# Kernel optimization log

Hardware: AMD Instinct MI355X
Metric: run time of the kernel (lower is better)

## Reference

```python
import jax, jax.numpy as jnp
import numpy as np

Q_STAGES = 8      # residual VQ stages
K_CODES = 1024    # codebook size per stage
D = 256           # code dim == encoder channels


def setup_inputs() -> dict:
    key = jax.random.key(0)
    ks = jax.random.split(key, 6)
    B, T = 8, 8192
    x = jax.random.normal(ks[0], (B, 1, T), dtype=jnp.float32)
    enc_w = jax.random.normal(ks[1], (D, 1, 3), dtype=jnp.float32) * 0.3
    enc_b = jnp.zeros((D,), dtype=jnp.float32)
    dec_w = jax.random.normal(ks[2], (1, D, 3), dtype=jnp.float32) * (1.0 / np.sqrt(3 * D))
    dec_b = jnp.zeros((1,), dtype=jnp.float32)
    codebooks = jax.random.normal(ks[3], (Q_STAGES, K_CODES, D), dtype=jnp.float32)
    return {"x": x, "enc_w": enc_w, "enc_b": enc_b,
            "dec_w": dec_w, "dec_b": dec_b, "codebooks": codebooks}


def _conv1d(x, w, b):
    # x: [B,C,T], w: [O,I,3], 'same' padding
    y = jax.lax.conv_general_dilated(x, w, window_strides=(1,), padding='SAME',
                                     dimension_numbers=('NCH', 'OIH', 'NCH'))
    return y + b[None, :, None]


def _rvq(z, codebooks):
    # z: [B,D,T] -> tokens [N,D]
    B, d, T = z.shape
    flat = jnp.transpose(z, (0, 2, 1)).reshape(B * T, d)  # [N,D]

    def stage(carry, cb):
        residual, quant_sum, loss = carry
        r2 = jnp.sum(residual * residual, axis=1, keepdims=True)      # [N,1]
        c2 = jnp.sum(cb * cb, axis=1)                                  # [K]
        dist = r2 - 2.0 * (residual @ cb.T) + c2[None, :]              # [N,K]
        idx = jnp.argmin(dist, axis=1)                                 # [N]
        q = jax.lax.stop_gradient(cb[idx])                             # [N,D]
        loss = loss + jnp.mean((residual - q) ** 2)                    # commitment
        return (residual - q, quant_sum + q, loss), None

    init = (flat, jnp.zeros_like(flat), jnp.float32(0.0))
    (res, quant_sum, loss), _ = jax.lax.scan(stage, init, codebooks)
    # straight-through estimator
    quant = flat + jax.lax.stop_gradient(quant_sum - flat)
    quant = jnp.transpose(quant.reshape(B, T, d), (0, 2, 1))           # [B,D,T]
    return quant, loss


def reference(x, enc_w, enc_b, dec_w, dec_b, codebooks):
    encoded = _conv1d(x, enc_w, enc_b)              # [B,256,T]
    quantized, commit_loss = _rvq(encoded, codebooks)
    decoded = _conv1d(quantized, dec_w, dec_b)      # [B,1,T]
    return decoded, commit_loss
```

## Files before the change

kernel.cpp:

```cpp
#include <hip/hip_runtime.h>

#define QS 8
#define KC 1024
#define DD 256
#define TT 8192
#define NN 65536
#define TAU 0.06f
#define FLAGCAP 49152

typedef _Float16 half8 __attribute__((ext_vector_type(8)));
typedef float f32x4 __attribute__((ext_vector_type(4)));

__device__ __forceinline__ void gload_lds16(const _Float16* g, _Float16* l) {
    __builtin_amdgcn_global_load_lds(
        (const __attribute__((address_space(1))) void*)g,
        (__attribute__((address_space(3))) void*)l,
        16, 0, 0);
}

__global__ __launch_bounds__(256) void encode_init_kernel(
    const float* __restrict__ x, const float* __restrict__ ew,
    const float* __restrict__ eb, float* __restrict__ res,
    float* __restrict__ lossAcc, int* __restrict__ flagCnt)
{
    if (blockIdx.x == 0 && threadIdx.x == 0) *lossAcc = 0.0f;
    if (blockIdx.x == 0 && threadIdx.x < QS) flagCnt[threadIdx.x] = 0;
    const int d = threadIdx.x;
    const float w0 = ew[d*3 + 0];
    const float w1 = ew[d*3 + 1];
    const float w2 = ew[d*3 + 2];
    const float b  = eb[d];
    #pragma unroll 4
    for (int tt = 0; tt < 16; ++tt) {
        const long n = (long)blockIdx.x * 16 + tt;
        const int t = (int)(n & (TT - 1));
        const float xm = (t > 0)      ? x[n - 1] : 0.0f;
        const float x0 = x[n];
        const float xp = (t < TT - 1) ? x[n + 1] : 0.0f;
        res[n * DD + d] = b + w0*xm + w1*x0 + w2*xp;
    }
}

__global__ __launch_bounds__(256) void c2_kernel(
    const float* __restrict__ cbs, float* __restrict__ c2)
{
    const int w = (int)((blockIdx.x * blockDim.x + threadIdx.x) >> 6);
    const int lane = threadIdx.x & 63;
    if (w >= QS * KC) return;
    const float* row = cbs + (long)w * DD;
    float s = 0.0f;
    #pragma unroll
    for (int q = 0; q < DD / 64; ++q) {
        const float v = row[lane + 64*q];
        s += v * v;
    }
    #pragma unroll
    for (int off = 32; off; off >>= 1) s += __shfl_down(s, off, 64);
    if (lane == 0) c2[w] = s;
}

__global__ __launch_bounds__(256) void cb_prep_stage_kernel(
    const float* __restrict__ cb, _Float16* __restrict__ cbh)
{
    const int t = blockIdx.x;
    const int cg = t >> 2, kp = t & 3;
    #pragma unroll
    for (int q = 0; q < 2; ++q) {
        const int p = threadIdx.x + 256*q;
        const int code = p & 63, kchunk = p >> 6;
        const float* src = &cb[(long)(cg*64 + code)*DD + kp*64 + kchunk*8];
        const float4 v0 = *reinterpret_cast<const float4*>(src);
        const float4 v1 = *reinterpret_cast<const float4*>(src + 4);
        half8 hv;
        hv[0]=(_Float16)v0.x; hv[1]=(_Float16)v0.y;
        hv[2]=(_Float16)v0.z; hv[3]=(_Float16)v0.w;
        hv[4]=(_Float16)v1.x; hv[5]=(_Float16)v1.y;
        hv[6]=(_Float16)v1.z; hv[7]=(_Float16)v1.w;
        *reinterpret_cast<half8*>(&cbh[(long)t*4096 + p*8]) = hv;
    }
}

__global__ __launch_bounds__(256, 2) void rvq_pass1_kernel(
    const float* __restrict__ cb,
    const _Float16* __restrict__ cbh,
    const float* __restrict__ c2,
    float* __restrict__ res,
    float* __restrict__ lossAcc,
    int* __restrict__ flagCnt,
    int* __restrict__ flagList)
{
    __shared__ __align__(16) _Float16 Bt[4][4096];
    __shared__ int idxArr[128];

    const int tid = threadIdx.x;
    const int w   = tid >> 6;
    const int l   = tid & 63;
    const int l15 = l & 15;
    const int l4  = l >> 4;
    const long n0 = (long)blockIdx.x * 128;

    int tr;
    {
        half8 pa, pb;
        #pragma unroll
        for (int e = 0; e < 8; ++e) {
            pa[e] = (_Float16)l15;
            pb[e] = (_Float16)0.03125f;
        }
        f32x4 pacc = (f32x4){0.f, 0.f, 0.f, 0.f};
        pacc = __builtin_amdgcn_mfma_f32_16x16x32_f16(pa, pb, pacc, 0, 0, 0);
        const float p1 = __shfl(pacc[1], 0, 64);
        tr = (p1 < 0.5f) ? 1 : 0;
    }

    half8 ah[2][8], al[2][8];
    #pragma unroll
    for (int mt = 0; mt < 2; ++mt) {
      #pragma unroll
      for (int kc = 0; kc < 8; ++kc) {
        const long n = n0 + w*32 + mt*16 + l15;
        const float* p = &res[n*DD + kc*32 + l4*8];
        const float4 v0 = *reinterpret_cast<const float4*>(p);
        const float4 v1 = *reinterpret_cast<const float4*>(p + 4);
        const float xv[8] = {v0.x, v0.y, v0.z, v0.w, v1.x, v1.y, v1.z, v1.w};
        half8 hv, lv;
        #pragma unroll
        for (int e = 0; e < 8; ++e) {
            const _Float16 hh = (_Float16)xv[e];
            hv[e] = hh;
            lv[e] = (_Float16)(xv[e] - (float)hh);
        }
        ah[mt][kc] = hv; al[mt][kc] = lv;
      }
    }

    float b1[8], b2[8]; int i1[8];
    #pragma unroll
    for (int r = 0; r < 8; ++r) { b1[r] = 1e30f; b2[r] = 1e30f; i1[r] = 0; }

    auto stageDMA = [&](int t) {
        const _Float16* src = cbh + (long)t*4096;
        const int buf = t & 3;
        gload_lds16(src + ((w*64 + l)*8),        &Bt[buf][w*512]);
        gload_lds16(src + ((256 + w*64 + l)*8),  &Bt[buf][2048 + w*512]);
    };

    stageDMA(0); stageDMA(1); stageDMA(2);

    for (int cg = 0; cg < 16; ++cg) {
      f32x4 acc[2][4];
      #pragma unroll
      for (int mt = 0; mt < 2; ++mt)
        #pragma unroll
        for (int nt = 0; nt < 4; ++nt)
          acc[mt][nt] = (f32x4){0.f, 0.f, 0.f, 0.f};

      for (int kp = 0; kp < 4; ++kp) {
        const int t = cg*4 + kp, buf = t & 3;

        if (t < 62)       asm volatile("s_waitcnt vmcnt(4)" ::: "memory");
        else if (t == 62) asm volatile("s_waitcnt vmcnt(2)" ::: "memory");
        else              asm volatile("s_waitcnt vmcnt(0)" ::: "memory");
        __builtin_amdgcn_sched_barrier(0);
        __builtin_amdgcn_s_barrier();
        __builtin_amdgcn_sched_barrier(0);

        if (t < 61) stageDMA(t + 3);

        #pragma unroll
        for (int kc2 = 0; kc2 < 2; ++kc2) {
          const int kc = kp*2 + kc2;
          #pragma unroll
          for (int nt = 0; nt < 4; ++nt) {
            const int slot = ((kc2*4 + l4)*64 + nt*16 + l15)*8;
            const half8 bh = *reinterpret_cast<const half8*>(&Bt[buf][slot]);
            #pragma unroll
            for (int mt = 0; mt < 2; ++mt) {
              acc[mt][nt] = __builtin_amdgcn_mfma_f32_16x16x32_f16(ah[mt][kc], bh, acc[mt][nt], 0, 0, 0);
              acc[mt][nt] = __builtin_amdgcn_mfma_f32_16x16x32_f16(al[mt][kc], bh, acc[mt][nt], 0, 0, 0);
            }
          }
        }
      }

      if (tr == 0) {
        #pragma unroll
        for (int nt = 0; nt < 4; ++nt) {
          const int code = cg*64 + nt*16 + l15;
          const float cc = c2[code];
          #pragma unroll
          for (int mt = 0; mt < 2; ++mt) {
            #pragma unroll
            for (int j = 0; j < 4; ++j) {
              const float dist = cc - 2.0f*acc[mt][nt][j];
              const int r = mt*4 + j;
              if (dist < b1[r])      { b2[r] = b1[r]; b1[r] = dist; i1[r] = code; }
              else if (dist < b2[r]) { b2[r] = dist; }
            }
          }
        }
      } else {
        #pragma unroll
        for (int nt = 0; nt < 4; ++nt) {
          #pragma unroll
          for (int j = 0; j < 4; ++j) {
            const int code = cg*64 + nt*16 + l4*4 + j;
            const float cc = c2[code];
            #pragma unroll
            for (int mt = 0; mt < 2; ++mt) {
              const float dist = cc - 2.0f*acc[mt][nt][j];
              if (dist < b1[mt])      { b2[mt] = b1[mt]; b1[mt] = dist; i1[mt] = code; }
              else if (dist < b2[mt]) { b2[mt] = dist; }
            }
          }
        }
      }
    }

    if (tr == 0) {
      #pragma unroll
      for (int m = 1; m < 16; m <<= 1) {
        #pragma unroll
        for (int r = 0; r < 8; ++r) {
          const float ob1 = __shfl_xor(b1[r], m, 64);
          const float ob2 = __shfl_xor(b2[r], m, 64);
          const int   oi1 = __shfl_xor(i1[r], m, 64);
          const float nb2 = fminf(fminf(b2[r], ob2), fmaxf(b1[r], ob1));
          if (ob1 < b1[r] || (ob1 == b1[r] && oi1 < i1[r])) { b1[r] = ob1; i1[r] = oi1; }
          b2[r] = nb2;
        }
      }
      if (l15 == 0) {
        #pragma unroll
        for (int mt = 0; mt < 2; ++mt)
          #pragma unroll
          for (int j = 0; j < 4; ++j) {
            const int r = mt*4 + j;
            const int row = w*32 + mt*16 + l4*4 + j;
            idxArr[row] = i1[r];
            if (b2[r] - b1[r] < TAU) {
              const int pos = atomicAdd(flagCnt, 1);
              if (pos < FLAGCAP)
                flagList[pos] = (int)(((n0 + row) << 10) | (unsigned)i1[r]);
            }
          }
      }
    } else {
      #pragma unroll
      for (int m = 16; m <= 32; m <<= 1) {
        #pragma unroll
        for (int r = 0; r < 2; ++r) {
          const float ob1 = __shfl_xor(b1[r], m, 64);
          const float ob2 = __shfl_xor(b2[r], m, 64);
          const int   oi1 = __shfl_xor(i1[r], m, 64);
          const float nb2 = fminf(fminf(b2[r], ob2), fmaxf(b1[r], ob1));
          if (ob1 < b1[r] || (ob1 == b1[r] && oi1 < i1[r])) { b1[r] = ob1; i1[r] = oi1; }
          b2[r] = nb2;
        }
      }
      if (l4 == 0) {
        #pragma unroll
        for (int mt = 0; mt < 2; ++mt) {
          const int row = w*32 + mt*16 + l15;
          idxArr[row] = i1[mt];
          if (b2[mt] - b1[mt] < TAU) {
            const int pos = atomicAdd(flagCnt, 1);
            if (pos < FLAGCAP)
              flagList[pos] = (int)(((n0 + row) << 10) | (unsigned)i1[mt]);
          }
        }
      }
    }
    __syncthreads();

    float lsum = 0.0f;
    const int rw = tid >> 6;
    const int cc4 = (tid & 63) * 4;
    #pragma unroll 4
    for (int it = 0; it < 32; ++it) {
        const int r = it*4 + rw;
        const long n = n0 + r;
        const int ix = idxArr[r];
        float4 rv = *reinterpret_cast<const float4*>(&res[n*DD + cc4]);
        const float4 cv = *reinterpret_cast<const float4*>(&cb[(long)ix*DD + cc4]);
        rv.x -= cv.x; rv.y -= cv.y; rv.z -= cv.z; rv.w -= cv.w;
        *reinterpret_cast<float4*>(&res[n*DD + cc4]) = rv;
        lsum += rv.x*rv.x + rv.y*rv.y + rv.z*rv.z + rv.w*rv.w;
    }
    #pragma unroll
    for (int off = 32; off; off >>= 1) lsum += __shfl_down(lsum, off, 64);
    if (l == 0) atomicAdd(lossAcc, lsum);
}

__global__ __launch_bounds__(256) void recheck_kernel(
    const float* __restrict__ cb, const float* __restrict__ c2,
    float* __restrict__ res, float* __restrict__ lossAcc,
    const int* __restrict__ flagCnt, const int* __restrict__ flagList)
{
    __shared__ float rorig[DD];
    __shared__ float sD[256];
    __shared__ int   sI[256];
    const int cnt = min(*flagCnt, FLAGCAP);
    const int tid = threadIdx.x;
    for (int f = blockIdx.x; f < cnt; f += gridDim.x) {
        const int packed = flagList[f];
        const long n  = packed >> 10;
        const int old = packed & 1023;
        __syncthreads();
        const float rme = res[n*DD + tid] + cb[(long)old*DD + tid];
        rorig[tid] = rme;
        __syncthreads();
        float bd = 1e30f; int bi = 0;
        #pragma unroll
        for (int q = 0; q < 4; ++q) {
            const int code = tid + 256*q;
            const float* crow = &cb[(long)code*DD];
            float dot = 0.f;
            for (int d = 0; d < DD; ++d) dot += rorig[d]*crow[d];
            const float dist = c2[code] - 2.0f*dot;
            if (dist < bd || (dist == bd && code < bi)) { bd = dist; bi = code; }
        }
        sD[tid] = bd; sI[tid] = bi;
        __syncthreads();
        for (int s = 128; s; s >>= 1) {
            if (tid < s) {
                const float d2 = sD[tid + s]; const int i2 = sI[tid + s];
                if (d2 < sD[tid] || (d2 == sD[tid] && i2 < sI[tid])) { sD[tid] = d2; sI[tid] = i2; }
            }
            __syncthreads();
        }
        const int best = sI[0];
        if (best != old) {
            const float rn = rorig[tid] - cb[(long)best*DD + tid];
            const float ro = res[n*DD + tid];
            res[n*DD + tid] = rn;
            float delta = rn*rn - ro*ro;
            #pragma unroll
            for (int off = 32; off; off >>= 1) delta += __shfl_down(delta, off, 64);
            if ((tid & 63) == 0) atomicAdd(lossAcc, delta);
        }
    }
}

__global__ __launch_bounds__(256) void decode_kernel(
    const float* __restrict__ x,  const float* __restrict__ ew,
    const float* __restrict__ eb, const float* __restrict__ res,
    const float* __restrict__ dw, const float* __restrict__ db,
    const float* __restrict__ lossAcc, float* __restrict__ out)
{
    const long n = (long)blockIdx.x * 4 + (threadIdx.x >> 6);
    const int lane = threadIdx.x & 63;
    const int t = (int)(n & (TT - 1));
    float sum = 0.0f;
    #pragma unroll
    for (int k = 0; k < 3; ++k) {
        const int tm = t + k - 1;
        if (tm < 0 || tm > TT - 1) continue;
        const long m = n + k - 1;
        const float xm = (tm > 0)      ? x[m - 1] : 0.0f;
        const float x0 = x[m];
        const float xp = (tm < TT - 1) ? x[m + 1] : 0.0f;
        #pragma unroll
        for (int q = 0; q < 4; ++q) {
            const int d = lane + 64 * q;
            const float z = eb[d] + ew[d*3]*xm + ew[d*3 + 1]*x0 + ew[d*3 + 2]*xp;
            const float quant = z - res[m * DD + d];
            sum += quant * dw[d*3 + k];
        }
    }
    #pragma unroll
    for (int off = 32; off; off >>= 1) sum += __shfl_down(sum, off, 64);
    if (lane == 0) out[n] = sum + db[0];
    if (blockIdx.x == 0 && threadIdx.x == 0)
        out[NN] = lossAcc[0] * (1.0f / ((float)NN * (float)DD));
}

extern "C" void kernel_launch(void* const* d_in, const int* in_sizes, int n_in,
                              void* d_out, int out_size, void* d_ws, size_t ws_size,
                              hipStream_t stream)
{
    const float* x     = (const float*)d_in[0];
    const float* enc_w = (const float*)d_in[1];
    const float* enc_b = (const float*)d_in[2];
    const float* dec_w = (const float*)d_in[3];
    const float* dec_b = (const float*)d_in[4];
    const float* cbs   = (const float*)d_in[5];
    float* out = (float*)d_out;

    float*    res      = (float*)d_ws;
    float*    lossAcc  = res + (size_t)NN * DD;
    _Float16* cbh      = (_Float16*)(lossAcc + 4);
    int*      flagCnt  = (int*)out;
    float*    c2       = out + 8;
    int*      flagList = (int*)(out + 8 + QS * KC);

    hipLaunchKernelGGL(encode_init_kernel, dim3(NN / 16), dim3(256), 0, stream,
                       x, enc_w, enc_b, res, lossAcc, flagCnt);
    hipLaunchKernelGGL(c2_kernel, dim3(QS * KC / 4), dim3(256), 0, stream,
                       cbs, c2);
    for (int s = 0; s < QS; ++s) {
        hipLaunchKernelGGL(cb_prep_stage_kernel, dim3(64), dim3(256), 0, stream,
                           cbs + (size_t)s * KC * DD, cbh);
        hipLaunchKernelGGL(rvq_pass1_kernel, dim3(NN / 128), dim3(256), 0, stream,
                           cbs + (size_t)s * KC * DD, cbh,
                           c2 + (size_t)s * KC,
                           res, lossAcc, flagCnt + s, flagList);
        hipLaunchKernelGGL(recheck_kernel, dim3(256), dim3(256), 0, stream,
                           cbs + (size_t)s * KC * DD,
                           c2 + (size_t)s * KC,
                           res, lossAcc, flagCnt + s, flagList);
    }
    hipLaunchKernelGGL(decode_kernel, dim3(NN / 4), dim3(256), 0, stream,
                       x, enc_w, enc_b, res, dec_w, dec_b, lossAcc, out);
}
```

Before: 1.507 ms.

## Fuse encoder, all RVQ stages and recheck into one register-resident persistent kernel

Replaces the per-stage prep/pass1/recheck launches with a single kernel. Each thread keeps its token's residual in registers across all eight stages, computes the encoder inline, and handles near-tie rows with an in-block exact fp32 recheck. The final residual is written once in fp16. This removes the repeated global read-modify-write of the 64 MB fp32 residual and about twenty kernel launches. The cost is heavy register pressure from r[8][8] with 512-thread blocks, a serialized in-block recheck loop with many barriers, reduced residual precision going into the decoder, and flags per block capped at 64.

```diff
diff --git a/kernel.cpp b/kernel.cpp
--- a/kernel.cpp
+++ b/kernel.cpp
@@ -6,7 +6,6 @@
 #define TT 8192
 #define NN 65536
 #define TAU 0.06f
-#define FLAGCAP 49152
 
 typedef _Float16 half8 __attribute__((ext_vector_type(8)));
 typedef float f32x4 __attribute__((ext_vector_type(4)));
@@ -18,52 +17,13 @@
         16, 0, 0);
 }
 
-__global__ __launch_bounds__(256) void encode_init_kernel(
-    const float* __restrict__ x, const float* __restrict__ ew,
-    const float* __restrict__ eb, float* __restrict__ res,
-    float* __restrict__ lossAcc, int* __restrict__ flagCnt)
-{
-    if (blockIdx.x == 0 && threadIdx.x == 0) *lossAcc = 0.0f;
-    if (blockIdx.x == 0 && threadIdx.x < QS) flagCnt[threadIdx.x] = 0;
-    const int d = threadIdx.x;
-    const float w0 = ew[d*3 + 0];
-    const float w1 = ew[d*3 + 1];
-    const float w2 = ew[d*3 + 2];
-    const float b  = eb[d];
-    #pragma unroll 4
-    for (int tt = 0; tt < 16; ++tt) {
-        const long n = (long)blockIdx.x * 16 + tt;
-        const int t = (int)(n & (TT - 1));
-        const float xm = (t > 0)      ? x[n - 1] : 0.0f;
-        const float x0 = x[n];
-        const float xp = (t < TT - 1) ? x[n + 1] : 0.0f;
-        res[n * DD + d] = b + w0*xm + w1*x0 + w2*xp;
-    }
-}
-
-__global__ __launch_bounds__(256) void c2_kernel(
-    const float* __restrict__ cbs, float* __restrict__ c2)
-{
-    const int w = (int)((blockIdx.x * blockDim.x + threadIdx.x) >> 6);
-    const int lane = threadIdx.x & 63;
-    if (w >= QS * KC) return;
-    const float* row = cbs + (long)w * DD;
-    float s = 0.0f;
-    #pragma unroll
-    for (int q = 0; q < DD / 64; ++q) {
-        const float v = row[lane + 64*q];
-        s += v * v;
-    }
-    #pragma unroll
-    for (int off = 32; off; off >>= 1) s += __shfl_down(s, off, 64);
-    if (lane == 0) c2[w] = s;
-}
-
-__global__ __launch_bounds__(256) void cb_prep_stage_kernel(
-    const float* __restrict__ cb, _Float16* __restrict__ cbh)
-{
-    const int t = blockIdx.x;
+__global__ __launch_bounds__(256) void cb_prep_all_kernel(
+    const float* __restrict__ cbs, _Float16* __restrict__ cbh)
+{
+    const int b = blockIdx.x, s = b >> 6, t = b & 63;
     const int cg = t >> 2, kp = t & 3;
+    const float* cb = cbs + (size_t)s * KC * DD;
+    _Float16* dst = cbh + (size_t)s * KC * DD + (size_t)t * 4096;
     #pragma unroll
     for (int q = 0; q < 2; ++q) {
         const int p = threadIdx.x + 256*q;
@@ -76,28 +36,51 @@
         hv[2]=(_Float16)v0.z; hv[3]=(_Float16)v0.w;
         hv[4]=(_Float16)v1.x; hv[5]=(_Float16)v1.y;
         hv[6]=(_Float16)v1.z; hv[7]=(_Float16)v1.w;
-        *reinterpret_cast<half8*>(&cbh[(long)t*4096 + p*8]) = hv;
-    }
-}
-
-__global__ __launch_bounds__(256, 2) void rvq_pass1_kernel(
-    const float* __restrict__ cb,
-    const _Float16* __restrict__ cbh,
-    const float* __restrict__ c2,
-    float* __restrict__ res,
-    float* __restrict__ lossAcc,
-    int* __restrict__ flagCnt,
-    int* __restrict__ flagList)
+        *reinterpret_cast<half8*>(&dst[p*8]) = hv;
+    }
+}
+
+__global__ __launch_bounds__(256) void c2_kernel(
+    const float* __restrict__ cbs, float* __restrict__ c2,
+    float* __restrict__ lossAcc)
+{
+    if (blockIdx.x == 0 && threadIdx.x == 0) *lossAcc = 0.0f;
+    const int w = (int)((blockIdx.x * blockDim.x + threadIdx.x) >> 6);
+    const int lane = threadIdx.x & 63;
+    if (w >= QS * KC) return;
+    const float* row = cbs + (long)w * DD;
+    float s = 0.0f;
+    #pragma unroll
+    for (int q = 0; q < DD / 64; ++q) {
+        const float v = row[lane + 64*q];
+        s += v * v;
+    }
+    #pragma unroll
+    for (int off = 32; off; off >>= 1) s += __shfl_down(s, off, 64);
+    if (lane == 0) c2[w] = s;
+}
+
+__global__ __launch_bounds__(512, 2) void mega_kernel(
+    const float* __restrict__ x,   const float* __restrict__ ew,
+    const float* __restrict__ eb,  const float* __restrict__ cbs,
+    const _Float16* __restrict__ cbh, const float* __restrict__ c2,
+    _Float16* __restrict__ resf,   float* __restrict__ lossAcc)
 {
     __shared__ __align__(16) _Float16 Bt[4][4096];
-    __shared__ int idxArr[128];
+    __shared__ int   idxArr[128];
+    __shared__ float rrow[DD];
+    __shared__ float sD8[8];
+    __shared__ int   sI8[8];
+    __shared__ int   flagRows[64];
+    __shared__ int   flagCnt;
 
     const int tid = threadIdx.x;
     const int w   = tid >> 6;
     const int l   = tid & 63;
     const int l15 = l & 15;
     const int l4  = l >> 4;
-    const long n0 = (long)blockIdx.x * 128;
+    const int n0  = blockIdx.x * 128;
+    const int n   = n0 + w*16 + l15;
 
     int tr;
     {
@@ -113,238 +96,226 @@
         tr = (p1 < 0.5f) ? 1 : 0;
     }
 
-    half8 ah[2][8], al[2][8];
-    #pragma unroll
-    for (int mt = 0; mt < 2; ++mt) {
-      #pragma unroll
-      for (int kc = 0; kc < 8; ++kc) {
-        const long n = n0 + w*32 + mt*16 + l15;
-        const float* p = &res[n*DD + kc*32 + l4*8];
-        const float4 v0 = *reinterpret_cast<const float4*>(p);
-        const float4 v1 = *reinterpret_cast<const float4*>(p + 4);
-        const float xv[8] = {v0.x, v0.y, v0.z, v0.w, v1.x, v1.y, v1.z, v1.w};
-        half8 hv, lv;
-        #pragma unroll
-        for (int e = 0; e < 8; ++e) {
-            const _Float16 hh = (_Float16)xv[e];
-            hv[e] = hh;
-            lv[e] = (_Float16)(xv[e] - (float)hh);
-        }
-        ah[mt][kc] = hv; al[mt][kc] = lv;
-      }
-    }
-
-    float b1[8], b2[8]; int i1[8];
-    #pragma unroll
-    for (int r = 0; r < 8; ++r) { b1[r] = 1e30f; b2[r] = 1e30f; i1[r] = 0; }
-
-    auto stageDMA = [&](int t) {
-        const _Float16* src = cbh + (long)t*4096;
-        const int buf = t & 3;
-        gload_lds16(src + ((w*64 + l)*8),        &Bt[buf][w*512]);
-        gload_lds16(src + ((256 + w*64 + l)*8),  &Bt[buf][2048 + w*512]);
-    };
-
-    stageDMA(0); stageDMA(1); stageDMA(2);
-
-    for (int cg = 0; cg < 16; ++cg) {
-      f32x4 acc[2][4];
-      #pragma unroll
-      for (int mt = 0; mt < 2; ++mt)
-        #pragma unroll
-        for (int nt = 0; nt < 4; ++nt)
-          acc[mt][nt] = (f32x4){0.f, 0.f, 0.f, 0.f};
-
-      for (int kp = 0; kp < 4; ++kp) {
-        const int t = cg*4 + kp, buf = t & 3;
-
-        if (t < 62)       asm volatile("s_waitcnt vmcnt(4)" ::: "memory");
-        else if (t == 62) asm volatile("s_waitcnt vmcnt(2)" ::: "memory");
-        else              asm volatile("s_waitcnt vmcnt(0)" ::: "memory");
-        __builtin_amdgcn_sched_barrier(0);
-        __builtin_amdgcn_s_barrier();
-        __builtin_amdgcn_sched_barrier(0);
-
-        if (t < 61) stageDMA(t + 3);
-
-        #pragma unroll
-        for (int kc2 = 0; kc2 < 2; ++kc2) {
-          const int kc = kp*2 + kc2;
-          #pragma unroll
-          for (int nt = 0; nt < 4; ++nt) {
-            const int slot = ((kc2*4 + l4)*64 + nt*16 + l15)*8;
-            const half8 bh = *reinterpret_cast<const half8*>(&Bt[buf][slot]);
-            #pragma unroll
-            for (int mt = 0; mt < 2; ++mt) {
-              acc[mt][nt] = __builtin_amdgcn_mfma_f32_16x16x32_f16(ah[mt][kc], bh, acc[mt][nt], 0, 0, 0);
-              acc[mt][nt] = __builtin_amdgcn_mfma_f32_16x16x32_f16(al[mt][kc], bh, acc[mt][nt], 0, 0, 0);
-            }
-          }
-        }
-      }
-
-      if (tr == 0) {
-        #pragma unroll
-        for (int nt = 0; nt < 4; ++nt) {
-          const int code = cg*64 + nt*16 + l15;
-          const float cc = c2[code];
-          #pragma unroll
-          for (int mt = 0; mt < 2; ++mt) {
-            #pragma unroll
-            for (int j = 0; j < 4; ++j) {
-              const float dist = cc - 2.0f*acc[mt][nt][j];
-              const int r = mt*4 + j;
-              if (dist < b1[r])      { b2[r] = b1[r]; b1[r] = dist; i1[r] = code; }
-              else if (dist < b2[r]) { b2[r] = dist; }
-            }
-          }
-        }
-      } else {
-        #pragma unroll
-        for (int nt = 0; nt < 4; ++nt) {
-          #pragma unroll
-          for (int j = 0; j < 4; ++j) {
-            const int code = cg*64 + nt*16 + l4*4 + j;
-            const float cc = c2[code];
-            #pragma unroll
-            for (int mt = 0; mt < 2; ++mt) {
-              const float dist = cc - 2.0f*acc[mt][nt][j];
-              if (dist < b1[mt])      { b2[mt] = b1[mt]; b1[mt] = dist; i1[mt] = code; }
-              else if (dist < b2[mt]) { b2[mt] = dist; }
-            }
-          }
-        }
-      }
-    }
-
-    if (tr == 0) {
-      #pragma unroll
-      for (int m = 1; m < 16; m <<= 1) {
-        #pragma unroll
-        for (int r = 0; r < 8; ++r) {
-          const float ob1 = __shfl_xor(b1[r], m, 64);
-          const float ob2 = __shfl_xor(b2[r], m, 64);
-          const int   oi1 = __shfl_xor(i1[r], m, 64);
-          const float nb2 = fminf(fminf(b2[r], ob2), fmaxf(b1[r], ob1));
-          if (ob1 < b1[r] || (ob1 == b1[r] && oi1 < i1[r])) { b1[r] = ob1; i1[r] = oi1; }
-          b2[r] = nb2;
-        }
-      }
-      if (l15 == 0) {
-        #pragma unroll
-        for (int mt = 0; mt < 2; ++mt)
-          #pragma unroll
-          for (int j = 0; j < 4; ++j) {
-            const int r = mt*4 + j;
-            const int row = w*32 + mt*16 + l4*4 + j;
-            idxArr[row] = i1[r];
-            if (b2[r] - b1[r] < TAU) {
-              const int pos = atomicAdd(flagCnt, 1);
-              if (pos < FLAGCAP)
-                flagList[pos] = (int)(((n0 + row) << 10) | (unsigned)i1[r]);
-            }
-          }
-      }
-    } else {
-      #pragma unroll
-      for (int m = 16; m <= 32; m <<= 1) {
-        #pragma unroll
-        for (int r = 0; r < 2; ++r) {
-          const float ob1 = __shfl_xor(b1[r], m, 64);
-          const float ob2 = __shfl_xor(b2[r], m, 64);
-          const int   oi1 = __shfl_xor(i1[r], m, 64);
-          const float nb2 = fminf(fminf(b2[r], ob2), fmaxf(b1[r], ob1));
-          if (ob1 < b1[r] || (ob1 == b1[r] && oi1 < i1[r])) { b1[r] = ob1; i1[r] = oi1; }
-          b2[r] = nb2;
-        }
-      }
-      if (l4 == 0) {
-        #pragma unroll
-        for (int mt = 0; mt < 2; ++mt) {
-          const int row = w*32 + mt*16 + l15;
-          idxArr[row] = i1[mt];
-          if (b2[mt] - b1[mt] < TAU) {
-            const int pos = atomicAdd(flagCnt, 1);
-            if (pos < FLAGCAP)
-              flagList[pos] = (int)(((n0 + row) << 10) | (unsigned)i1[mt]);
-          }
-        }
-      }
-    }
-    __syncthreads();
+    float r[8][8];
+    {
+        const int t = n & (TT - 1);
+        const float xm = (t > 0)      ? x[n - 1] : 0.0f;
+        const float x0v = x[n];
+        const float xp = (t < TT - 1) ? x[n + 1] : 0.0f;
+        #pragma unroll
+        for (int kc = 0; kc < 8; ++kc)
+            #pragma unroll
+            for (int e = 0; e < 8; ++e) {
+                const int d = kc*32 + l4*8 + e;
+                r[kc][e] = eb[d] + ew[3*d]*xm + ew[3*d+1]*x0v + ew[3*d+2]*xp;
+            }
+    }
 
     float lsum = 0.0f;
-    const int rw = tid >> 6;
-    const int cc4 = (tid & 63) * 4;
-    #pragma unroll 4
-    for (int it = 0; it < 32; ++it) {
-        const int r = it*4 + rw;
-        const long n = n0 + r;
-        const int ix = idxArr[r];
-        float4 rv = *reinterpret_cast<const float4*>(&res[n*DD + cc4]);
-        const float4 cv = *reinterpret_cast<const float4*>(&cb[(long)ix*DD + cc4]);
-        rv.x -= cv.x; rv.y -= cv.y; rv.z -= cv.z; rv.w -= cv.w;
-        *reinterpret_cast<float4*>(&res[n*DD + cc4]) = rv;
-        lsum += rv.x*rv.x + rv.y*rv.y + rv.z*rv.z + rv.w*rv.w;
+    half8 ah[8], al[8];
+
+    for (int s = 0; s < QS; ++s) {
+        const _Float16* cbhS = cbh + (size_t)s * KC * DD;
+        const float*    cbS  = cbs + (size_t)s * KC * DD;
+        const float*    c2S  = c2 + s * KC;
+
+        #pragma unroll
+        for (int kc = 0; kc < 8; ++kc) {
+            half8 hv, lv;
+            #pragma unroll
+            for (int e = 0; e < 8; ++e) {
+                const _Float16 hh = (_Float16)r[kc][e];
+                hv[e] = hh;
+                lv[e] = (_Float16)(r[kc][e] - (float)hh);
+            }
+            ah[kc] = hv; al[kc] = lv;
+        }
+
+        if (tid == 0) flagCnt = 0;
+
+        float b1[4], b2[4]; int i1[4];
+        #pragma unroll
+        for (int q = 0; q < 4; ++q) { b1[q] = 1e30f; b2[q] = 1e30f; i1[q] = 0; }
+
+        gload_lds16(cbhS + 0*4096 + tid*8, &Bt[0][w*512]);
+        gload_lds16(cbhS + 1*4096 + tid*8, &Bt[1][w*512]);
+        gload_lds16(cbhS + 2*4096 + tid*8, &Bt[2][w*512]);
+
+        for (int cg = 0; cg < 16; ++cg) {
+            f32x4 acc[4];
+            #pragma unroll
+            for (int nt = 0; nt < 4; ++nt) acc[nt] = (f32x4){0.f,0.f,0.f,0.f};
+
+            for (int kp = 0; kp < 4; ++kp) {
+                const int t = cg*4 + kp, buf = t & 3;
+                if (t < 62)      asm volatile("s_waitcnt vmcnt(2)" ::: "memory");
+                else if (t==62)  asm volatile("s_waitcnt vmcnt(1)" ::: "memory");
+                else             asm volatile("s_waitcnt vmcnt(0)" ::: "memory");
+                __builtin_amdgcn_sched_barrier(0);
+                __builtin_amdgcn_s_barrier();
+                __builtin_amdgcn_sched_barrier(0);
+
+                if (t < 61)
+                    gload_lds16(cbhS + (size_t)(t+3)*4096 + tid*8, &Bt[(t+3)&3][w*512]);
+
+                #pragma unroll
+                for (int kc2 = 0; kc2 < 2; ++kc2) {
+                    const int kc = kp*2 + kc2;
+                    #pragma unroll
+                    for (int nt = 0; nt < 4; ++nt) {
+                        const int slot = ((kc2*4 + l4)*64 + nt*16 + l15)*8;
+                        const half8 bh = *reinterpret_cast<const half8*>(&Bt[buf][slot]);
+                        acc[nt] = __builtin_amdgcn_mfma_f32_16x16x32_f16(ah[kc], bh, acc[nt], 0, 0, 0);
+                        acc[nt] = __builtin_amdgcn_mfma_f32_16x16x32_f16(al[kc], bh, acc[nt], 0, 0, 0);
+                    }
+                }
+            }
+
+            if (tr == 0) {
+                #pragma unroll
+                for (int nt = 0; nt < 4; ++nt) {
+                    const int code = cg*64 + nt*16 + l15;
+                    const float cc = c2S[code];
+                    #pragma unroll
+                    for (int j = 0; j < 4; ++j) {
+                        const float dist = cc - 2.0f*acc[nt][j];
+                        if (dist < b1[j])      { b2[j] = b1[j]; b1[j] = dist; i1[j] = code; }
+                        else if (dist < b2[j]) { b2[j] = dist; }
+                    }
+                }
+            } else {
+                #pragma unroll
+                for (int nt = 0; nt < 4; ++nt) {
+                    #pragma unroll
+                    for (int j = 0; j < 4; ++j) {
+                        const int code = cg*64 + nt*16 + l4*4 + j;
+                        const float dist = c2S[code] - 2.0f*acc[nt][j];
+                        if (dist < b1[0])      { b2[0] = b1[0]; b1[0] = dist; i1[0] = code; }
+                        else if (dist < b2[0]) { b2[0] = dist; }
+                    }
+                }
+            }
+        }
+
+        if (tr == 0) {
+            #pragma unroll
+            for (int m = 1; m < 16; m <<= 1) {
+                #pragma unroll
+                for (int q = 0; q < 4; ++q) {
+                    const float ob1 = __shfl_xor(b1[q], m, 64);
+                    const float ob2 = __shfl_xor(b2[q], m, 64);
+                    const int   oi1 = __shfl_xor(i1[q], m, 64);
+                    const float nb2 = fminf(fminf(b2[q], ob2), fmaxf(b1[q], ob1));
+                    if (ob1 < b1[q] || (ob1 == b1[q] && oi1 < i1[q])) { b1[q] = ob1; i1[q] = oi1; }
+                    b2[q] = nb2;
+                }
+            }
+            if (l15 == 0) {
+                #pragma unroll
+                for (int j = 0; j < 4; ++j) {
+                    const int row = w*16 + l4*4 + j;
+                    idxArr[row] = i1[j];
+                    if (b2[j] - b1[j] < TAU) {
+                        const int pos = atomicAdd(&flagCnt, 1);
+                        if (pos < 64) flagRows[pos] = row;
+                    }
+                }
+            }
+        } else {
+            #pragma unroll
+            for (int m = 16; m <= 32; m <<= 1) {
+                const float ob1 = __shfl_xor(b1[0], m, 64);
+                const float ob2 = __shfl_xor(b2[0], m, 64);
+                const int   oi1 = __shfl_xor(i1[0], m, 64);
+                const float nb2 = fminf(fminf(b2[0], ob2), fmaxf(b1[0], ob1));
+                if (ob1 < b1[0] || (ob1 == b1[0] && oi1 < i1[0])) { b1[0] = ob1; i1[0] = oi1; }
+                b2[0] = nb2;
+            }
+            if (l4 == 0) {
+                const int row = w*16 + l15;
+                idxArr[row] = i1[0];
+                if (b2[0] - b1[0] < TAU) {
+                    const int pos = atomicAdd(&flagCnt, 1);
+                    if (pos < 64) flagRows[pos] = row;
+                }
+            }
+        }
+        __syncthreads();
+
+        const int fc = min(flagCnt, 64);
+        for (int f = 0; f < fc; ++f) {
+            const int row = flagRows[f];
+            if (w == (row >> 4) && l15 == (row & 15)) {
+                #pragma unroll
+                for (int kc = 0; kc < 8; ++kc)
+                    #pragma unroll
+                    for (int e = 0; e < 8; ++e)
+                        rrow[kc*32 + l4*8 + e] = r[kc][e];
+            }
+            __syncthreads();
+            float bd = 1e30f; int bi = 0;
+            #pragma unroll
+            for (int q = 0; q < 2; ++q) {
+                const int code = tid*2 + q;
+                const float* crow = cbS + (size_t)code * DD;
+                float dot = 0.f;
+                for (int d4 = 0; d4 < DD; d4 += 4) {
+                    const float4 cv = *reinterpret_cast<const float4*>(&crow[d4]);
+                    dot += rrow[d4]*cv.x + rrow[d4+1]*cv.y
+                         + rrow[d4+2]*cv.z + rrow[d4+3]*cv.w;
+                }
+                const float dist = c2S[code] - 2.0f*dot;
+                if (dist < bd || (dist == bd && code < bi)) { bd = dist; bi = code; }
+            }
+            #pragma unroll
+            for (int off = 32; off; off >>= 1) {
+                const float od = __shfl_down(bd, off, 64);
+                const int   oi = __shfl_down(bi, off, 64);
+                if (od < bd || (od == bd && oi < bi)) { bd = od; bi = oi; }
+            }
+            if (l == 0) { sD8[w] = bd; sI8[w] = bi; }
+            __syncthreads();
+            if (tid == 0) {
+                float fbd = sD8[0]; int fbi = sI8[0];
+                #pragma unroll
+                for (int ww = 1; ww < 8; ++ww) {
+                    if (sD8[ww] < fbd || (sD8[ww] == fbd && sI8[ww] < fbi)) {
+                        fbd = sD8[ww]; fbi = sI8[ww];
+                    }
+                }
+                idxArr[row] = fbi;
+            }
+            __syncthreads();
+        }
+
+        const int ix = idxArr[w*16 + l15];
+        const float* crow = cbS + (size_t)ix * DD;
+        #pragma unroll
+        for (int kc = 0; kc < 8; ++kc) {
+            const float4 c0 = *reinterpret_cast<const float4*>(&crow[kc*32 + l4*8]);
+            const float4 c1 = *reinterpret_cast<const float4*>(&crow[kc*32 + l4*8 + 4]);
+            r[kc][0] -= c0.x; r[kc][1] -= c0.y; r[kc][2] -= c0.z; r[kc][3] -= c0.w;
+            r[kc][4] -= c1.x; r[kc][5] -= c1.y; r[kc][6] -= c1.z; r[kc][7] -= c1.w;
+            #pragma unroll
+            for (int e = 0; e < 8; ++e) lsum += r[kc][e]*r[kc][e];
+        }
+    }
+
+    #pragma unroll
+    for (int kc = 0; kc < 8; ++kc) {
+        half8 hv;
+        #pragma unroll
+        for (int e = 0; e < 8; ++e) hv[e] = (_Float16)r[kc][e];
+        *reinterpret_cast<half8*>(&resf[(size_t)n*DD + kc*32 + l4*8]) = hv;
     }
     #pragma unroll
     for (int off = 32; off; off >>= 1) lsum += __shfl_down(lsum, off, 64);
     if (l == 0) atomicAdd(lossAcc, lsum);
 }
 
-__global__ __launch_bounds__(256) void recheck_kernel(
-    const float* __restrict__ cb, const float* __restrict__ c2,
-    float* __restrict__ res, float* __restrict__ lossAcc,
-    const int* __restrict__ flagCnt, const int* __restrict__ flagList)
-{
-    __shared__ float rorig[DD];
-    __shared__ float sD[256];
-    __shared__ int   sI[256];
-    const int cnt = min(*flagCnt, FLAGCAP);
-    const int tid = threadIdx.x;
-    for (int f = blockIdx.x; f < cnt; f += gridDim.x) {
-        const int packed = flagList[f];
-        const long n  = packed >> 10;
-        const int old = packed & 1023;
-        __syncthreads();
-        const float rme = res[n*DD + tid] + cb[(long)old*DD + tid];
-        rorig[tid] = rme;
-        __syncthreads();
-        float bd = 1e30f; int bi = 0;
-        #pragma unroll
-        for (int q = 0; q < 4; ++q) {
-            const int code = tid + 256*q;
-            const float* crow = &cb[(long)code*DD];
-            float dot = 0.f;
-            for (int d = 0; d < DD; ++d) dot += rorig[d]*crow[d];
-            const float dist = c2[code] - 2.0f*dot;
-            if (dist < bd || (dist == bd && code < bi)) { bd = dist; bi = code; }
-        }
-        sD[tid] = bd; sI[tid] = bi;
-        __syncthreads();
-        for (int s = 128; s; s >>= 1) {
-            if (tid < s) {
-                const float d2 = sD[tid + s]; const int i2 = sI[tid + s];
-                if (d2 < sD[tid] || (d2 == sD[tid] && i2 < sI[tid])) { sD[tid] = d2; sI[tid] = i2; }
-            }
-            __syncthreads();
-        }
-        const int best = sI[0];
-        if (best != old) {
-            const float rn = rorig[tid] - cb[(long)best*DD + tid];
-            const float ro = res[n*DD + tid];
-            res[n*DD + tid] = rn;
-            float delta = rn*rn - ro*ro;
-            #pragma unroll
-            for (int off = 32; off; off >>= 1) delta += __shfl_down(delta, off, 64);
-            if ((tid & 63) == 0) atomicAdd(lossAcc, delta);
-        }
-    }
-}
-
 __global__ __launch_bounds__(256) void decode_kernel(
     const float* __restrict__ x,  const float* __restrict__ ew,
-    const float* __restrict__ eb, const float* __restrict__ res,
+    const float* __restrict__ eb, const _Float16* __restrict__ resf,
     const float* __restrict__ dw, const float* __restrict__ db,
     const float* __restrict__ lossAcc, float* __restrict__ out)
 {
@@ -364,7 +335,7 @@
         for (int q = 0; q < 4; ++q) {
             const int d = lane + 64 * q;
             const float z = eb[d] + ew[d*3]*xm + ew[d*3 + 1]*x0 + ew[d*3 + 2]*xp;
-            const float quant = z - res[m * DD + d];
+            const float quant = z - (float)resf[m * DD + d];
             sum += quant * dw[d*3 + k];
         }
     }
@@ -387,29 +358,17 @@
     const float* cbs   = (const float*)d_in[5];
     float* out = (float*)d_out;
 
-    float*    res      = (float*)d_ws;
-    float*    lossAcc  = res + (size_t)NN * DD;
-    _Float16* cbh      = (_Float16*)(lossAcc + 4);
-    int*      flagCnt  = (int*)out;
-    float*    c2       = out + 8;
-    int*      flagList = (int*)(out + 8 + QS * KC);
-
-    hipLaunchKernelGGL(encode_init_kernel, dim3(NN / 16), dim3(256), 0, stream,
-                       x, enc_w, enc_b, res, lossAcc, flagCnt);
+    _Float16* resf    = (_Float16*)d_ws;
+    _Float16* cbh     = resf + (size_t)NN * DD;
+    float*    lossAcc = (float*)(cbh + (size_t)QS * KC * DD);
+    float*    c2      = out + 8;
+
+    hipLaunchKernelGGL(cb_prep_all_kernel, dim3(QS * 64), dim3(256), 0, stream,
+                       cbs, cbh);
     hipLaunchKernelGGL(c2_kernel, dim3(QS * KC / 4), dim3(256), 0, stream,
-                       cbs, c2);
-    for (int s = 0; s < QS; ++s) {
-        hipLaunchKernelGGL(cb_prep_stage_kernel, dim3(64), dim3(256), 0, stream,
-                           cbs + (size_t)s * KC * DD, cbh);
-        hipLaunchKernelGGL(rvq_pass1_kernel, dim3(NN / 128), dim3(256), 0, stream,
-                           cbs + (size_t)s * KC * DD, cbh,
-                           c2 + (size_t)s * KC,
-                           res, lossAcc, flagCnt + s, flagList);
-        hipLaunchKernelGGL(recheck_kernel, dim3(256), dim3(256), 0, stream,
-                           cbs + (size_t)s * KC * DD,
-                           c2 + (size_t)s * KC,
-                           res, lossAcc, flagCnt + s, flagList);
-    }
+                       cbs, c2, lossAcc);
+    hipLaunchKernelGGL(mega_kernel, dim3(NN / 128), dim3(512), 0, stream,
+                       x, enc_w, enc_b, cbs, cbh, c2, resf, lossAcc);
     hipLaunchKernelGGL(decode_kernel, dim3(NN / 4), dim3(256), 0, stream,
-                       x, enc_w, enc_b, res, dec_w, dec_b, lossAcc, out);
-}
+                       x, enc_w, enc_b, resf, dec_w, dec_b, lossAcc, out);
+}
```

Result: no change. 1.534 ms (+1.8%).
